# Performance work log

Hardware: AMD Instinct MI355X
Metric: run time of the kernel (lower is better)

Reference implementation:

```python
import jax, jax.numpy as jnp
import numpy as np

N = 20000      # num_nodes
E = 320000     # num_edges
T = 24         # seq_len
SD = 16        # static_dim
DD = 8         # dynamic_dim
HID = 128      # hidden_dim
HEADS = 4
DPH = HID // HEADS  # per-head dim (GATConv out_channels = hidden_dim // heads)
L = 3          # num_gnn_layers
LN_EPS = 1e-5


def setup_inputs() -> dict:
    key = jax.random.key(0)
    ks = jax.random.split(key, 16)
    f = lambda i, shape, s=0.1: jax.random.normal(ks[i], shape, jnp.float32) * s
    return {
        "x_static": f(0, (N, SD), 1.0),
        "x_dynamic": f(1, (T, N, DD), 1.0),
        "edge_index": jax.random.randint(ks[2], (2, E), 0, N),
        "proj_W": f(3, (SD + DD, HID)),
        "proj_b": jnp.zeros((HID,), jnp.float32),
        "gat_W": f(4, (L, HID, HID)),
        "att_src": f(5, (L, HEADS, DPH)),
        "att_dst": f(6, (L, HEADS, DPH)),
        "gat_b": jnp.zeros((L, HID), jnp.float32),
        "ln_g": jnp.ones((L, HID), jnp.float32),
        "ln_b": jnp.zeros((L, HID), jnp.float32),
        "lstm_Wih0": f(7, (4 * HID, HID)),
        "lstm_Whh0": f(8, (4 * HID, HID)),
        "lstm_bih0": jnp.zeros((4 * HID,), jnp.float32),
        "lstm_bhh0": jnp.zeros((4 * HID,), jnp.float32),
        "lstm_Wih1": f(9, (4 * HID, HID)),
        "lstm_Whh1": f(10, (4 * HID, HID)),
        "lstm_bih1": jnp.zeros((4 * HID,), jnp.float32),
        "lstm_bhh1": jnp.zeros((4 * HID,), jnp.float32),
        "out_W1": f(11, (HID, HID // 2)),
        "out_b1": jnp.zeros((HID // 2,), jnp.float32),
        "out_W2": f(12, (HID // 2, 1)),
        "out_b2": jnp.zeros((1,), jnp.float32),
    }


def _gat_layer(h, src, dst, W, a_s, a_d, b, g, beta):
    """PyG GATConv (self-loops already in src/dst) + residual + LayerNorm + ReLU."""
    Nn = h.shape[0]
    xp = (h @ W).reshape(Nn, HEADS, DPH)                # [N, H, D]
    a_src = (xp * a_s).sum(-1)                          # [N, H]
    a_dst = (xp * a_d).sum(-1)                          # [N, H]
    e = jax.nn.leaky_relu(a_src[src] + a_dst[dst], 0.2)  # [E', H]
    m = jax.ops.segment_max(e, dst, num_segments=Nn)
    ex = jnp.exp(e - m[dst])
    denom = jax.ops.segment_sum(ex, dst, num_segments=Nn)
    alpha = ex / (denom[dst] + 1e-16)                   # segment softmax over in-edges
    msg = xp[src] * alpha[:, :, None]                   # [E', H, D]
    out = jax.ops.segment_sum(msg, dst, num_segments=Nn).reshape(Nn, HID) + b
    out = out + h                                       # residual (dims match)
    mu = out.mean(-1, keepdims=True)
    var = ((out - mu) ** 2).mean(-1, keepdims=True)
    out = g * (out - mu) * jax.lax.rsqrt(var + LN_EPS) + beta
    return jax.nn.relu(out)


def _lstm_cell(x, h, c, Wih, Whh, bih, bhh):
    z = x @ Wih.T + h @ Whh.T + bih + bhh
    i, f, gg, o = jnp.split(z, 4, axis=-1)              # torch gate order i,f,g,o
    c = jax.nn.sigmoid(f) * c + jax.nn.sigmoid(i) * jnp.tanh(gg)
    h = jax.nn.sigmoid(o) * jnp.tanh(c)
    return h, c


def reference(x_static, x_dynamic, edge_index, proj_W, proj_b, gat_W, att_src,
              att_dst, gat_b, ln_g, ln_b, lstm_Wih0, lstm_Whh0, lstm_bih0,
              lstm_bhh0, lstm_Wih1, lstm_Whh1, lstm_bih1, lstm_bhh1,
              out_W1, out_b1, out_W2, out_b2):
    Nn = x_static.shape[0]
    loop = jnp.arange(Nn)
    src = jnp.concatenate([edge_index[0], loop])        # GATConv add_self_loops=True
    dst = jnp.concatenate([edge_index[1], loop])

    @jax.checkpoint
    def timestep(xd_t):
        h = jnp.concatenate([x_static, xd_t], axis=-1) @ proj_W + proj_b
        for l in range(L):
            h = _gat_layer(h, src, dst, gat_W[l], att_src[l], att_dst[l],
                           gat_b[l], ln_g[l], ln_b[l])
        return h

    h_seq = jax.lax.map(timestep, x_dynamic)            # [T, N, HID]

    def step(carry, x_t):
        h0, c0, h1, c1 = carry
        h0, c0 = _lstm_cell(x_t, h0, c0, lstm_Wih0, lstm_Whh0, lstm_bih0, lstm_bhh0)
        h1, c1 = _lstm_cell(h0, h1, c1, lstm_Wih1, lstm_Whh1, lstm_bih1, lstm_bhh1)
        return (h0, c0, h1, c1), None

    z = jnp.zeros((Nn, HID), x_static.dtype)
    (_, _, h1, _), _ = jax.lax.scan(step, (z, z, z, z), h_seq)
    pred = jax.nn.relu(h1 @ out_W1 + out_b1) @ out_W2 + out_b2
    return pred[:, 0]
```

## Files before the change

### kernel.cpp

```cpp
#include <hip/hip_runtime.h>
#include <hip/hip_bf16.h>
#include <math.h>

#define NN   20000
#define NE   320000
#define TT   24
#define SDIM 16
#define DDIM 8
#define HID  128
#define HEADS 4
#define DPH  32
#define NL   3
#define TC   2

typedef unsigned short u16;
typedef unsigned int   u32;
typedef __attribute__((ext_vector_type(8))) short  short8;
typedef __attribute__((ext_vector_type(4))) float  floatx4;

__device__ __forceinline__ u16 f2bf(float x) {
  u32 u = __float_as_uint(x);
  return (u16)((u + 0x7fff + ((u >> 16) & 1)) >> 16);
}
__device__ __forceinline__ float bf2f(u16 b) {
  return __uint_as_float(((u32)b) << 16);
}

__global__ void k_count(const int* __restrict__ dst, int* __restrict__ cnt) {
  int e = blockIdx.x * 256 + threadIdx.x;
  if (e < NE) atomicAdd(&cnt[dst[e]], 1);
}

__global__ __launch_bounds__(1024) void k_scan(const int* __restrict__ cnt,
    int* __restrict__ rowptr, int* __restrict__ cursor) {
  __shared__ int sh[1024];
  int tid = threadIdx.x;
  const int CH = 20;
  int base = tid * CH;
  int local[CH];
  int s = 0;
  #pragma unroll
  for (int i = 0; i < CH; i++) {
    int idx = base + i;
    int v = (idx < NN) ? cnt[idx] : 0;
    local[i] = s;
    s += v;
  }
  sh[tid] = s;
  __syncthreads();
  for (int off = 1; off < 1024; off <<= 1) {
    int tv = (tid >= off) ? sh[tid - off] : 0;
    __syncthreads();
    sh[tid] += tv;
    __syncthreads();
  }
  int pre = (tid > 0) ? sh[tid - 1] : 0;
  #pragma unroll
  for (int i = 0; i < CH; i++) {
    int idx = base + i;
    if (idx < NN) { int e = pre + local[i]; rowptr[idx] = e; cursor[idx] = e; }
  }
  if (tid == 1023) rowptr[NN] = sh[1023];
}

__global__ void k_fill(const int* __restrict__ src, const int* __restrict__ dst,
    int* __restrict__ cursor, int* __restrict__ col) {
  int e = blockIdx.x * 256 + threadIdx.x;
  if (e < NE) {
    int pos = atomicAdd(&cursor[dst[e]], 1);
    col[pos] = src[e];
  }
}

__global__ void k_prepw_lstm(const float* __restrict__ Wih, const float* __restrict__ Whh,
    u16* __restrict__ Bt) {
  int idx = blockIdx.x * 256 + threadIdx.x;
  if (idx < 512 * 256) {
    int jp = idx >> 8, k = idx & 255;
    int c = jp >> 2, g = jp & 3;
    int j = g * 128 + c;
    float v = (k < 128) ? Wih[(size_t)j * 128 + k] : Whh[(size_t)j * 128 + (k - 128)];
    Bt[idx] = f2bf(v);
  }
}
__global__ void k_prepb(const float* __restrict__ bih0, const float* __restrict__ bhh0,
    const float* __restrict__ bih1, const float* __restrict__ bhh1,
    float* __restrict__ bs01) {
  int t = threadIdx.x;
  const float* bih = blockIdx.x ? bih1 : bih0;
  const float* bhh = blockIdx.x ? bhh1 : bhh0;
  int c = t >> 2, g = t & 3;
  bs01[blockIdx.x * 512 + t] = bih[g * 128 + c] + bhh[g * 128 + c];
}
__global__ void k_prepw_gat(const float* __restrict__ gatW, u16* __restrict__ Btg) {
  int idx = blockIdx.x * 256 + threadIdx.x;
  if (idx < NL * 128 * 128) {
    int l = idx >> 14, r = idx & 16383;
    int n = r >> 7, k = r & 127;
    Btg[idx] = f2bf(gatW[(size_t)l * 16384 + k * 128 + n]);
  }
}

__global__ __launch_bounds__(256) void k_proj(const float* __restrict__ xs,
    const float* __restrict__ xdt, const float* __restrict__ W,
    const float* __restrict__ b, u16* __restrict__ hbf) {
  __shared__ float Ws[24 * HID];
  __shared__ float xin[16][24];
  int tid = threadIdx.x;
  int tc = blockIdx.y;
  for (int i = tid; i < 24 * HID; i += 256) Ws[i] = W[i];
  int n0 = blockIdx.x * 16;
  for (int i = tid; i < 16 * 24; i += 256) {
    int r = i / 24, c = i % 24;
    int n = n0 + r;
    xin[r][c] = (c < SDIM) ? xs[(size_t)n * SDIM + c]
                           : xdt[(size_t)tc * NN * DDIM + (size_t)n * DDIM + (c - SDIM)];
  }
  __syncthreads();
  int ch = tid & 127, rb = (tid >> 7) * 8;
  for (int r = rb; r < rb + 8; r++) {
    float acc = b[ch];
    #pragma unroll
    for (int k = 0; k < 24; k++) acc = fmaf(xin[r][k], Ws[k * HID + ch], acc);
    hbf[((size_t)tc * NN + n0 + r) * HID + ch] = f2bf(acc);
  }
}

#define TBM 128
#define TBN 64
#define TBK 64

__global__ __launch_bounds__(256) void k_bgemm_gat(const u16* __restrict__ A,
    const u16* __restrict__ Bt, const float* __restrict__ as_,
    const float* __restrict__ ad_, u16* __restrict__ xpbf,
    float* __restrict__ asrc, float* __restrict__ adst, int M) {
  __shared__ u16 As[TBM][TBK + 8];
  __shared__ u16 Bs[TBN][TBK + 8];
  int tid = threadIdx.x;
  int wid = tid >> 6, lane = tid & 63;
  int wr = wid >> 1, wc = wid & 1;
  int lrow = lane & 15, lgrp = lane >> 4;
  int row0 = blockIdx.x * TBM, col0 = blockIdx.y * TBN;
  floatx4 acc[4][2] = {};
  for (int k0 = 0; k0 < 128; k0 += TBK) {
    #pragma unroll
    for (int i = 0; i < 4; i++) {
      int idx = tid + i * 256;
      int r = idx >> 3, g = idx & 7;
      int gr = row0 + r;
      short8 v = {};
      if (gr < M) v = *(const short8*)(A + (size_t)gr * 128 + k0 + g * 8);
      *(short8*)&As[r][g * 8] = v;
    }
    #pragma unroll
    for (int i = 0; i < 2; i++) {
      int idx = tid + i * 256;
      int r = idx >> 3, g = idx & 7;
      *(short8*)&Bs[r][g * 8] = *(const short8*)(Bt + (size_t)(col0 + r) * 128 + k0 + g * 8);
    }
    __syncthreads();
    #pragma unroll
    for (int kk = 0; kk < TBK; kk += 32) {
      short8 bfr[2];
      #pragma unroll
      for (int n = 0; n < 2; n++)
        bfr[n] = *(const short8*)&Bs[wc * 32 + n * 16 + lrow][kk + lgrp * 8];
      #pragma unroll
      for (int m = 0; m < 4; m++) {
        short8 af = *(const short8*)&As[wr * 64 + m * 16 + lrow][kk + lgrp * 8];
        acc[m][0] = __builtin_amdgcn_mfma_f32_16x16x32_bf16(af, bfr[0], acc[m][0], 0, 0, 0);
        acc[m][1] = __builtin_amdgcn_mfma_f32_16x16x32_bf16(af, bfr[1], acc[m][1], 0, 0, 0);
      }
    }
    __syncthreads();
  }
  int head = (col0 >> 5) + wc;
  float as0 = as_[head * 32 + lrow], as1 = as_[head * 32 + 16 + lrow];
  float ad0 = ad_[head * 32 + lrow], ad1 = ad_[head * 32 + 16 + lrow];
  #pragma unroll
  for (int m = 0; m < 4; m++) {
    #pragma unroll
    for (int r = 0; r < 4; r++) {
      int grow = row0 + wr * 64 + m * 16 + lgrp * 4 + r;
      float v0 = acc[m][0][r], v1 = acc[m][1][r];
      if (grow < M) {
        xpbf[(size_t)grow * HID + col0 + wc * 32 + lrow]      = f2bf(v0);
        xpbf[(size_t)grow * HID + col0 + wc * 32 + 16 + lrow] = f2bf(v1);
      }
      float ps = v0 * as0 + v1 * as1;
      float pd = v0 * ad0 + v1 * ad1;
      #pragma unroll
      for (int off = 1; off < 16; off <<= 1) {
        ps += __shfl_xor(ps, off);
        pd += __shfl_xor(pd, off);
      }
      if (lrow == 0 && grow < M) {
        asrc[grow * HEADS + head] = ps;
        adst[grow * HEADS + head] = pd;
      }
    }
  }
}

__global__ __launch_bounds__(256) void k_aggr(const u16* __restrict__ xpbf,
    u16* __restrict__ hbf, const float* __restrict__ asrc,
    const float* __restrict__ adst, const int* __restrict__ rowptr,
    const int* __restrict__ col, const float* __restrict__ bias,
    const float* __restrict__ lng, const float* __restrict__ lnb) {
  int wid = threadIdx.x >> 6, lane = threadIdx.x & 63;
  int n = blockIdx.x * 4 + wid;
  int node = n, base = 0;
  if (n >= NN) { node = n - NN; base = NN; }
  int hh = lane >> 4;
  float ad = adst[n * HEADS + hh];
  float e0 = asrc[n * HEADS + hh] + ad;
  e0 = (e0 > 0.f) ? e0 : 0.2f * e0;
  float m = e0, den = 1.f;
  u32 xv = ((const u32*)(xpbf + (size_t)n * HID))[lane];
  float mg0 = bf2f((u16)(xv & 0xffff)), mg1 = bf2f((u16)(xv >> 16));
  int rs = rowptr[node], re = rowptr[node + 1];
  int j = rs;
  for (; j + 4 <= re; j += 4) {
    int r0 = base + col[j],     r1 = base + col[j + 1];
    int r2 = base + col[j + 2], r3 = base + col[j + 3];
    float ev0 = asrc[r0 * HEADS + hh] + ad;
    float ev1 = asrc[r1 * HEADS + hh] + ad;
    float ev2 = asrc[r2 * HEADS + hh] + ad;
    float ev3 = asrc[r3 * HEADS + hh] + ad;
    u32 x0 = ((const u32*)(xpbf + (size_t)r0 * HID))[lane];
    u32 x1 = ((const u32*)(xpbf + (size_t)r1 * HID))[lane];
    u32 x2 = ((const u32*)(xpbf + (size_t)r2 * HID))[lane];
    u32 x3 = ((const u32*)(xpbf + (size_t)r3 * HID))[lane];
    ev0 = (ev0 > 0.f) ? ev0 : 0.2f * ev0;
    ev1 = (ev1 > 0.f) ? ev1 : 0.2f * ev1;
    ev2 = (ev2 > 0.f) ? ev2 : 0.2f * ev2;
    ev3 = (ev3 > 0.f) ? ev3 : 0.2f * ev3;
    float mn = fmaxf(fmaxf(m, fmaxf(ev0, ev1)), fmaxf(ev2, ev3));
    float sc = __expf(m - mn);
    float w0 = __expf(ev0 - mn);
    float w1 = __expf(ev1 - mn);
    float w2 = __expf(ev2 - mn);
    float w3 = __expf(ev3 - mn);
    den = den * sc + ((w0 + w1) + (w2 + w3));
    mg0 = mg0 * sc + w0 * bf2f((u16)(x0 & 0xffff)) + w1 * bf2f((u16)(x1 & 0xffff))
                   + w2 * bf2f((u16)(x2 & 0xffff)) + w3 * bf2f((u16)(x3 & 0xffff));
    mg1 = mg1 * sc + w0 * bf2f((u16)(x0 >> 16))    + w1 * bf2f((u16)(x1 >> 16))
                   + w2 * bf2f((u16)(x2 >> 16))    + w3 * bf2f((u16)(x3 >> 16));
    m = mn;
  }
  for (; j < re; j++) {
    int r0 = base + col[j];
    float ev = asrc[r0 * HEADS + hh] + ad;
    ev = (ev > 0.f) ? ev : 0.2f * ev;
    u32 x2 = ((const u32*)(xpbf + (size_t)r0 * HID))[lane];
    float mn = fmaxf(m, ev);
    float sc = __expf(m - mn);
    float w  = __expf(ev - mn);
    den = den * sc + w;
    mg0 = mg0 * sc + w * bf2f((u16)(x2 & 0xffff));
    mg1 = mg1 * sc + w * bf2f((u16)(x2 >> 16));
    m = mn;
  }
  float inv = 1.f / (den + 1e-16f);
  int c0 = lane * 2;
  size_t hoff = (size_t)n * HID + c0;
  u32 hv = *(const u32*)(hbf + hoff);
  float o0 = mg0 * inv + bias[c0]     + bf2f((u16)(hv & 0xffff));
  float o1 = mg1 * inv + bias[c0 + 1] + bf2f((u16)(hv >> 16));
  float s2 = o0 + o1;
  #pragma unroll
  for (int off = 32; off; off >>= 1) s2 += __shfl_xor(s2, off);
  float mu = s2 * (1.f / HID);
  float d0 = o0 - mu, d1 = o1 - mu;
  float v2 = d0 * d0 + d1 * d1;
  #pragma unroll
  for (int off = 32; off; off >>= 1) v2 += __shfl_xor(v2, off);
  float rstd = rsqrtf(v2 * (1.f / HID) + 1e-5f);
  o0 = lng[c0] * d0 * rstd + lnb[c0];
  o1 = lng[c0 + 1] * d1 * rstd + lnb[c0 + 1];
  o0 = fmaxf(o0, 0.f);
  o1 = fmaxf(o1, 0.f);
  *(u32*)(hbf + hoff) = (u32)f2bf(o0) | ((u32)f2bf(o1) << 16);
}

__global__ __launch_bounds__(256) void k_bgemm_lstm(const u16* __restrict__ A0,
    const u16* __restrict__ A1, const u16* __restrict__ Bt,
    const float* __restrict__ bs, float* __restrict__ cst,
    u16* __restrict__ hout, int M) {
  __shared__ __align__(16) char smem[34816];
  u16 (*As)[TBK + 8] = (u16(*)[TBK + 8])smem;
  u16 (*Bs)[TBK + 8] = (u16(*)[TBK + 8])(smem + TBM * (TBK + 8) * 2);
  float (*zs)[68] = (float(*)[68])smem;
  int tid = threadIdx.x;
  int wid = tid >> 6, lane = tid & 63;
  int wr = wid >> 1, wc = wid & 1;
  int lrow = lane & 15, lgrp = lane >> 4;
  int row0 = blockIdx.x * TBM, col0 = blockIdx.y * TBN;
  floatx4 acc[4][2] = {};
  for (int k0 = 0; k0 < 256; k0 += TBK) {
    const u16* Ap = (k0 < 128) ? A0 : A1;
    int kb = k0 & 127;
    #pragma unroll
    for (int i = 0; i < 4; i++) {
      int idx = tid + i * 256;
      int r = idx >> 3, g = idx & 7;
      int gr = row0 + r;
      short8 v = {};
      if (gr < M) v = *(const short8*)(Ap + (size_t)gr * 128 + kb + g * 8);
      *(short8*)&As[r][g * 8] = v;
    }
    #pragma unroll
    for (int i = 0; i < 2; i++) {
      int idx = tid + i * 256;
      int r = idx >> 3, g = idx & 7;
      *(short8*)&Bs[r][g * 8] = *(const short8*)(Bt + (size_t)(col0 + r) * 256 + k0 + g * 8);
    }
    __syncthreads();
    #pragma unroll
    for (int kk = 0; kk < TBK; kk += 32) {
      short8 bfr[2];
      #pragma unroll
      for (int n = 0; n < 2; n++)
        bfr[n] = *(const short8*)&Bs[wc * 32 + n * 16 + lrow][kk + lgrp * 8];
      #pragma unroll
      for (int m = 0; m < 4; m++) {
        short8 af = *(const short8*)&As[wr * 64 + m * 16 + lrow][kk + lgrp * 8];
        acc[m][0] = __builtin_amdgcn_mfma_f32_16x16x32_bf16(af, bfr[0], acc[m][0], 0, 0, 0);
        acc[m][1] = __builtin_amdgcn_mfma_f32_16x16x32_bf16(af, bfr[1], acc[m][1], 0, 0, 0);
      }
    }
    __syncthreads();
  }
  #pragma unroll
  for (int m = 0; m < 4; m++)
    #pragma unroll
    for (int n = 0; n < 2; n++)
      #pragma unroll
      for (int r = 0; r < 4; r++)
        zs[wr * 64 + m * 16 + lgrp * 4 + r][wc * 32 + n * 16 + lrow] = acc[m][n][r];
  __syncthreads();
  int ch0 = blockIdx.y * 16;
  #pragma unroll
  for (int it = 0; it < 8; it++) {
    int o = tid + it * 256;
    int r = o >> 4, lc = o & 15;
    int grow = row0 + r;
    if (grow < M) {
      float4 zi = *(float4*)&zs[r][lc * 4];
      int ch = ch0 + lc;
      size_t gi = (size_t)grow * HID + ch;
      float ii = zi.x + bs[4 * ch + 0];
      float ff = zi.y + bs[4 * ch + 1];
      float gg = zi.z + bs[4 * ch + 2];
      float oo = zi.w + bs[4 * ch + 3];
      float si = 1.f / (1.f + __expf(-ii));
      float sf = 1.f / (1.f + __expf(-ff));
      float so = 1.f / (1.f + __expf(-oo));
      float tg = tanhf(gg);
      float cn = sf * cst[gi] + si * tg;
      cst[gi] = cn;
      hout[gi] = f2bf(so * tanhf(cn));
    }
  }
}

__global__ __launch_bounds__(64) void k_mlp(const u16* __restrict__ h1,
    const float* __restrict__ W1, const float* __restrict__ b1,
    const float* __restrict__ W2, const float* __restrict__ b2,
    float* __restrict__ out) {
  int n = blockIdx.x, j = threadIdx.x;
  const u16* hr = h1 + (size_t)n * HID;
  float acc = b1[j];
  #pragma unroll 8
  for (int k = 0; k < HID; k++) acc = fmaf(bf2f(hr[k]), W1[(size_t)k * 64 + j], acc);
  acc = fmaxf(acc, 0.f);
  float p = acc * W2[j];
  #pragma unroll
  for (int off = 32; off; off >>= 1) p += __shfl_xor(p, off);
  if (j == 0) out[n] = p + b2[0];
}

extern "C" void kernel_launch(void* const* d_in, const int* in_sizes, int n_in,
                              void* d_out, int out_size, void* d_ws, size_t ws_size,
                              hipStream_t stream) {
  const float* xs    = (const float*)d_in[0];
  const float* xd    = (const float*)d_in[1];
  const int*   ei    = (const int*)d_in[2];
  const float* projW = (const float*)d_in[3];
  const float* projb = (const float*)d_in[4];
  const float* gatW  = (const float*)d_in[5];
  const float* attS  = (const float*)d_in[6];
  const float* attD  = (const float*)d_in[7];
  const float* gatb  = (const float*)d_in[8];
  const float* lng   = (const float*)d_in[9];
  const float* lnb   = (const float*)d_in[10];
  const float* Wih0  = (const float*)d_in[11];
  const float* Whh0  = (const float*)d_in[12];
  const float* bih0  = (const float*)d_in[13];
  const float* bhh0  = (const float*)d_in[14];
  const float* Wih1  = (const float*)d_in[15];
  const float* Whh1  = (const float*)d_in[16];
  const float* bih1  = (const float*)d_in[17];
  const float* bhh1  = (const float*)d_in[18];
  const float* oW1   = (const float*)d_in[19];
  const float* ob1   = (const float*)d_in[20];
  const float* oW2   = (const float*)d_in[21];
  const float* ob2   = (const float*)d_in[22];
  float* out = (float*)d_out;

  char* w = (char*)d_ws;
  size_t off = 0;
  auto alloc = [&](size_t bytes) { void* p = w + off; off += (bytes + 255) & ~(size_t)255; return p; };
  u16*   hbf   = (u16*)  alloc((size_t)TC * NN * HID * 2);
  u16*   xpbf  = (u16*)  alloc((size_t)TC * NN * HID * 2);
  float* asrc  = (float*)alloc((size_t)TC * NN * HEADS * 4);
  float* adst  = (float*)alloc((size_t)TC * NN * HEADS * 4);
  float* c01   = (float*)alloc((size_t)2 * NN * HID * 4);
  float* c0 = c01, *c1 = c01 + (size_t)NN * HID;
  u16*   h0p   = (u16*)  alloc((size_t)2 * NN * HID * 2);
  u16*   h1p   = (u16*)  alloc((size_t)2 * NN * HID * 2);
  u16*   h0buf[2] = { h0p, h0p + (size_t)NN * HID };
  u16*   h1buf[2] = { h1p, h1p + (size_t)NN * HID };
  u16*   Wc0bf = (u16*)alloc((size_t)512 * 256 * 2);
  u16*   Wc1bf = (u16*)alloc((size_t)512 * 256 * 2);
  float* bs01  = (float*)alloc((size_t)1024 * 4);
  float* bs0 = bs01, *bs1 = bs01 + 512;
  u16*   gatWbf= (u16*)alloc((size_t)NL * 128 * 128 * 2);
  int* cnt    = (int*)alloc((size_t)NN * 4);
  int* rowptr = (int*)alloc((size_t)(NN + 1) * 4);
  int* cursor = (int*)alloc((size_t)NN * 4);
  int* col    = (int*)alloc((size_t)NE * 4);

  const int* esrc = ei;
  const int* edst = ei + NE;

  hipMemsetAsync(cnt, 0, (size_t)NN * 4, stream);
  k_count<<<(NE + 255) / 256, 256, 0, stream>>>(edst, cnt);
  k_scan<<<1, 1024, 0, stream>>>(cnt, rowptr, cursor);
  k_fill<<<(NE + 255) / 256, 256, 0, stream>>>(esrc, edst, cursor, col);

  k_prepw_lstm<<<(512 * 256) / 256, 256, 0, stream>>>(Wih0, Whh0, Wc0bf);
  k_prepw_lstm<<<(512 * 256) / 256, 256, 0, stream>>>(Wih1, Whh1, Wc1bf);
  k_prepb<<<2, 512, 0, stream>>>(bih0, bhh0, bih1, bhh1, bs01);
  k_prepw_gat<<<(NL * 128 * 128) / 256, 256, 0, stream>>>(gatW, gatWbf);
  hipMemsetAsync(c01, 0, (size_t)2 * NN * HID * 4, stream);
  hipMemsetAsync(h0buf[0], 0, (size_t)NN * HID * 2, stream);
  hipMemsetAsync(h1buf[0], 0, (size_t)NN * HID * 2, stream);

  const int gx  = (NN + TBM - 1) / TBM;
  const int gx2 = (TC * NN + TBM - 1) / TBM;
  for (int tcb = 0; tcb < TT / TC; tcb++) {
    k_proj<<<dim3(NN / 16, TC), 256, 0, stream>>>(
        xs, xd + (size_t)(tcb * TC) * NN * DDIM, projW, projb, hbf);
    for (int l = 0; l < NL; l++) {
      k_bgemm_gat<<<dim3(gx2, 2), 256, 0, stream>>>(
          hbf, gatWbf + (size_t)l * 128 * 128,
          attS + l * HEADS * DPH, attD + l * HEADS * DPH,
          xpbf, asrc, adst, TC * NN);
      k_aggr<<<TC * NN / 4, 256, 0, stream>>>(
          xpbf, hbf, asrc, adst, rowptr, col, gatb + (size_t)l * HID,
          lng + (size_t)l * HID, lnb + (size_t)l * HID);
    }
    for (int s2 = 0; s2 < TC; s2++) {
      int t = tcb * TC + s2;
      int pi = t & 1;
      k_bgemm_lstm<<<dim3(gx, 8), 256, 0, stream>>>(
          hbf + (size_t)s2 * NN * HID, h0buf[pi], Wc0bf, bs0, c0, h0buf[pi ^ 1], NN);
      k_bgemm_lstm<<<dim3(gx, 8), 256, 0, stream>>>(
          h0buf[pi ^ 1], h1buf[pi], Wc1bf, bs1, c1, h1buf[pi ^ 1], NN);
    }
  }

  k_mlp<<<NN, 64, 0, stream>>>(h1buf[0], oW1, ob1, oW2, ob2, out);
}
```

Baseline: 3.799 ms.

## Batch four timesteps per launch and compute edge weights in parallel per 16-edge chunk

The timestep batch factor goes from 2 to 4, so each launch processes more graph copies and the launch count drops. The aggregation kernel now splits each node's in-edges into chunks of 16. Each lane computes one edge's score, and the chunk's max and weight sum come from shuffle reductions. The weights are staged in shared memory and applied in a serial gather loop. This cuts the number of serial exp and max steps per edge, but adds shuffles, LDS traffic and per-lane work imbalance for nodes with few edges, and it enlarges the intermediate buffers.

```diff
diff --git a/kernel.cpp b/kernel.cpp
--- a/kernel.cpp
+++ b/kernel.cpp
@@ -11,7 +11,7 @@
 #define HEADS 4
 #define DPH  32
 #define NL   3
-#define TC   2
+#define TC   4
 
 typedef unsigned short u16;
 typedef unsigned int   u32;
@@ -207,11 +207,12 @@
     const float* __restrict__ adst, const int* __restrict__ rowptr,
     const int* __restrict__ col, const float* __restrict__ bias,
     const float* __restrict__ lng, const float* __restrict__ lnb) {
+  __shared__ float wls[4][64];
   int wid = threadIdx.x >> 6, lane = threadIdx.x & 63;
   int n = blockIdx.x * 4 + wid;
-  int node = n, base = 0;
-  if (n >= NN) { node = n - NN; base = NN; }
-  int hh = lane >> 4;
+  int tc = n / NN;
+  int node = n - tc * NN, base = tc * NN;
+  int hh = lane >> 4, lrow = lane & 15;
   float ad = adst[n * HEADS + hh];
   float e0 = asrc[n * HEADS + hh] + ad;
   e0 = (e0 > 0.f) ? e0 : 0.2f * e0;
@@ -219,47 +220,39 @@
   u32 xv = ((const u32*)(xpbf + (size_t)n * HID))[lane];
   float mg0 = bf2f((u16)(xv & 0xffff)), mg1 = bf2f((u16)(xv >> 16));
   int rs = rowptr[node], re = rowptr[node + 1];
-  int j = rs;
-  for (; j + 4 <= re; j += 4) {
-    int r0 = base + col[j],     r1 = base + col[j + 1];
-    int r2 = base + col[j + 2], r3 = base + col[j + 3];
-    float ev0 = asrc[r0 * HEADS + hh] + ad;
-    float ev1 = asrc[r1 * HEADS + hh] + ad;
-    float ev2 = asrc[r2 * HEADS + hh] + ad;
-    float ev3 = asrc[r3 * HEADS + hh] + ad;
-    u32 x0 = ((const u32*)(xpbf + (size_t)r0 * HID))[lane];
-    u32 x1 = ((const u32*)(xpbf + (size_t)r1 * HID))[lane];
-    u32 x2 = ((const u32*)(xpbf + (size_t)r2 * HID))[lane];
-    u32 x3 = ((const u32*)(xpbf + (size_t)r3 * HID))[lane];
-    ev0 = (ev0 > 0.f) ? ev0 : 0.2f * ev0;
-    ev1 = (ev1 > 0.f) ? ev1 : 0.2f * ev1;
-    ev2 = (ev2 > 0.f) ? ev2 : 0.2f * ev2;
-    ev3 = (ev3 > 0.f) ? ev3 : 0.2f * ev3;
-    float mn = fmaxf(fmaxf(m, fmaxf(ev0, ev1)), fmaxf(ev2, ev3));
+  for (int jt = rs; jt < re; jt += 16) {
+    int e = jt + lrow;
+    bool valid = e < re;
+    int s = 0;
+    float ev = -3.0e38f;
+    if (valid) {
+      s = base + col[e];
+      ev = asrc[s * HEADS + hh] + ad;
+      ev = (ev > 0.f) ? ev : 0.2f * ev;
+    }
+    float tm = ev;
+    #pragma unroll
+    for (int off = 1; off < 16; off <<= 1) tm = fmaxf(tm, __shfl_xor(tm, off));
+    float mn = fmaxf(m, tm);
     float sc = __expf(m - mn);
-    float w0 = __expf(ev0 - mn);
-    float w1 = __expf(ev1 - mn);
-    float w2 = __expf(ev2 - mn);
-    float w3 = __expf(ev3 - mn);
-    den = den * sc + ((w0 + w1) + (w2 + w3));
-    mg0 = mg0 * sc + w0 * bf2f((u16)(x0 & 0xffff)) + w1 * bf2f((u16)(x1 & 0xffff))
-                   + w2 * bf2f((u16)(x2 & 0xffff)) + w3 * bf2f((u16)(x3 & 0xffff));
-    mg1 = mg1 * sc + w0 * bf2f((u16)(x0 >> 16))    + w1 * bf2f((u16)(x1 >> 16))
-                   + w2 * bf2f((u16)(x2 >> 16))    + w3 * bf2f((u16)(x3 >> 16));
+    float w = valid ? __expf(ev - mn) : 0.f;
+    float ws = w;
+    #pragma unroll
+    for (int off = 1; off < 16; off <<= 1) ws += __shfl_xor(ws, off);
+    wls[wid][lrow * 4 + hh] = w;
+    den = den * sc + ws;
+    mg0 *= sc;
+    mg1 *= sc;
     m = mn;
-  }
-  for (; j < re; j++) {
-    int r0 = base + col[j];
-    float ev = asrc[r0 * HEADS + hh] + ad;
-    ev = (ev > 0.f) ? ev : 0.2f * ev;
-    u32 x2 = ((const u32*)(xpbf + (size_t)r0 * HID))[lane];
-    float mn = fmaxf(m, ev);
-    float sc = __expf(m - mn);
-    float w  = __expf(ev - mn);
-    den = den * sc + w;
-    mg0 = mg0 * sc + w * bf2f((u16)(x2 & 0xffff));
-    mg1 = mg1 * sc + w * bf2f((u16)(x2 >> 16));
-    m = mn;
+    int cnt = min(16, re - jt);
+    #pragma unroll 4
+    for (int k = 0; k < cnt; k++) {
+      int sk = __shfl(s, k, 16);
+      float wk = wls[wid][k * 4 + hh];
+      u32 xg = ((const u32*)(xpbf + (size_t)sk * HID))[lane];
+      mg0 = fmaf(wk, bf2f((u16)(xg & 0xffff)), mg0);
+      mg1 = fmaf(wk, bf2f((u16)(xg >> 16)), mg1);
+    }
   }
   float inv = 1.f / (den + 1e-16f);
   int c0 = lane * 2;
```

After: 4.033 ms. +6.1%, slower.

## Drop online-max softmax in GAT aggregation and batch four timesteps

Applied to the files above, without the earlier changes.

The aggregation kernel no longer tracks a running maximum with rescaling. It computes exp of the clamped logits directly and keeps four independent partial accumulators, which removes the serial dependency chain and the extra exp per chunk. The timestep batch factor TC goes from 2 to 4, so more timesteps are processed per launch, and node/base indexing is generalised to match. The clamp at 80 limits overflow, but small logits can lose precision relative to max-subtracted softmax.

```diff
diff --git a/kernel.cpp b/kernel.cpp
--- a/kernel.cpp
+++ b/kernel.cpp
@@ -11,7 +11,7 @@
 #define HEADS 4
 #define DPH  32
 #define NL   3
-#define TC   2
+#define TC   4
 
 typedef unsigned short u16;
 typedef unsigned int   u32;
@@ -209,58 +209,61 @@
     const float* __restrict__ lng, const float* __restrict__ lnb) {
   int wid = threadIdx.x >> 6, lane = threadIdx.x & 63;
   int n = blockIdx.x * 4 + wid;
-  int node = n, base = 0;
-  if (n >= NN) { node = n - NN; base = NN; }
+  int tc = n / NN;
+  int node = n - tc * NN, base = tc * NN;
   int hh = lane >> 4;
   float ad = adst[n * HEADS + hh];
   float e0 = asrc[n * HEADS + hh] + ad;
   e0 = (e0 > 0.f) ? e0 : 0.2f * e0;
-  float m = e0, den = 1.f;
+  float w0 = __expf(fminf(e0, 80.f));
   u32 xv = ((const u32*)(xpbf + (size_t)n * HID))[lane];
-  float mg0 = bf2f((u16)(xv & 0xffff)), mg1 = bf2f((u16)(xv >> 16));
+  float den0 = w0, den1 = 0.f, den2 = 0.f, den3 = 0.f;
+  float p00 = w0 * bf2f((u16)(xv & 0xffff)), p10 = 0.f, p20 = 0.f, p30 = 0.f;
+  float p01 = w0 * bf2f((u16)(xv >> 16)),    p11 = 0.f, p21 = 0.f, p31 = 0.f;
   int rs = rowptr[node], re = rowptr[node + 1];
   int j = rs;
   for (; j + 4 <= re; j += 4) {
-    int r0 = base + col[j],     r1 = base + col[j + 1];
-    int r2 = base + col[j + 2], r3 = base + col[j + 3];
-    float ev0 = asrc[r0 * HEADS + hh] + ad;
-    float ev1 = asrc[r1 * HEADS + hh] + ad;
-    float ev2 = asrc[r2 * HEADS + hh] + ad;
-    float ev3 = asrc[r3 * HEADS + hh] + ad;
-    u32 x0 = ((const u32*)(xpbf + (size_t)r0 * HID))[lane];
-    u32 x1 = ((const u32*)(xpbf + (size_t)r1 * HID))[lane];
-    u32 x2 = ((const u32*)(xpbf + (size_t)r2 * HID))[lane];
-    u32 x3 = ((const u32*)(xpbf + (size_t)r3 * HID))[lane];
+    int s0 = base + col[j],     s1 = base + col[j + 1];
+    int s2 = base + col[j + 2], s3 = base + col[j + 3];
+    float ev0 = asrc[s0 * HEADS + hh] + ad;
+    float ev1 = asrc[s1 * HEADS + hh] + ad;
+    float ev2 = asrc[s2 * HEADS + hh] + ad;
+    float ev3 = asrc[s3 * HEADS + hh] + ad;
+    u32 x0 = ((const u32*)(xpbf + (size_t)s0 * HID))[lane];
+    u32 x1 = ((const u32*)(xpbf + (size_t)s1 * HID))[lane];
+    u32 x2 = ((const u32*)(xpbf + (size_t)s2 * HID))[lane];
+    u32 x3 = ((const u32*)(xpbf + (size_t)s3 * HID))[lane];
     ev0 = (ev0 > 0.f) ? ev0 : 0.2f * ev0;
     ev1 = (ev1 > 0.f) ? ev1 : 0.2f * ev1;
     ev2 = (ev2 > 0.f) ? ev2 : 0.2f * ev2;
     ev3 = (ev3 > 0.f) ? ev3 : 0.2f * ev3;
-    float mn = fmaxf(fmaxf(m, fmaxf(ev0, ev1)), fmaxf(ev2, ev3));
-    float sc = __expf(m - mn);
-    float w0 = __expf(ev0 - mn);
-    float w1 = __expf(ev1 - mn);
-    float w2 = __expf(ev2 - mn);
-    float w3 = __expf(ev3 - mn);
-    den = den * sc + ((w0 + w1) + (w2 + w3));
-    mg0 = mg0 * sc + w0 * bf2f((u16)(x0 & 0xffff)) + w1 * bf2f((u16)(x1 & 0xffff))
-                   + w2 * bf2f((u16)(x2 & 0xffff)) + w3 * bf2f((u16)(x3 & 0xffff));
-    mg1 = mg1 * sc + w0 * bf2f((u16)(x0 >> 16))    + w1 * bf2f((u16)(x1 >> 16))
-                   + w2 * bf2f((u16)(x2 >> 16))    + w3 * bf2f((u16)(x3 >> 16));
-    m = mn;
+    float w0e = __expf(fminf(ev0, 80.f));
+    float w1e = __expf(fminf(ev1, 80.f));
+    float w2e = __expf(fminf(ev2, 80.f));
+    float w3e = __expf(fminf(ev3, 80.f));
+    den0 += w0e; den1 += w1e; den2 += w2e; den3 += w3e;
+    p00 = fmaf(w0e, bf2f((u16)(x0 & 0xffff)), p00);
+    p10 = fmaf(w1e, bf2f((u16)(x1 & 0xffff)), p10);
+    p20 = fmaf(w2e, bf2f((u16)(x2 & 0xffff)), p20);
+    p30 = fmaf(w3e, bf2f((u16)(x3 & 0xffff)), p30);
+    p01 = fmaf(w0e, bf2f((u16)(x0 >> 16)), p01);
+    p11 = fmaf(w1e, bf2f((u16)(x1 >> 16)), p11);
+    p21 = fmaf(w2e, bf2f((u16)(x2 >> 16)), p21);
+    p31 = fmaf(w3e, bf2f((u16)(x3 >> 16)), p31);
   }
   for (; j < re; j++) {
-    int r0 = base + col[j];
-    float ev = asrc[r0 * HEADS + hh] + ad;
+    int s0 = base + col[j];
+    float ev = asrc[s0 * HEADS + hh] + ad;
     ev = (ev > 0.f) ? ev : 0.2f * ev;
-    u32 x2 = ((const u32*)(xpbf + (size_t)r0 * HID))[lane];
-    float mn = fmaxf(m, ev);
-    float sc = __expf(m - mn);
-    float w  = __expf(ev - mn);
-    den = den * sc + w;
-    mg0 = mg0 * sc + w * bf2f((u16)(x2 & 0xffff));
-    mg1 = mg1 * sc + w * bf2f((u16)(x2 >> 16));
-    m = mn;
-  }
+    u32 x0 = ((const u32*)(xpbf + (size_t)s0 * HID))[lane];
+    float w = __expf(fminf(ev, 80.f));
+    den0 += w;
+    p00 = fmaf(w, bf2f((u16)(x0 & 0xffff)), p00);
+    p01 = fmaf(w, bf2f((u16)(x0 >> 16)), p01);
+  }
+  float den = (den0 + den1) + (den2 + den3);
+  float mg0 = (p00 + p10) + (p20 + p30);
+  float mg1 = (p01 + p11) + (p21 + p31);
   float inv = 1.f / (den + 1e-16f);
   int c0 = lane * 2;
   size_t hoff = (size_t)n * HID + c0;
```

Result: faster. 3.499 ms (-7.9%).
